# Optimization experiments

Hardware: AMD Instinct MI355X
Metric: run time of the kernel (lower is better)

The kernel has to match this reference:

```python
import jax, jax.numpy as jnp
import numpy as np

N = 50000
E = 800000
IN_F = 128
HID_F = 128
OUT_F = 128
BN_EPS = 1e-5


def make_quaternion_mul(kernel):
    # kernel: [d_in//4, d_out]; returns hamilton: [d_in, d_out]
    r, i, j, k = jnp.split(kernel, 4, axis=1)
    r2 = jnp.concatenate([r, -i, -j, -k], axis=0)
    i2 = jnp.concatenate([i, r, -k, j], axis=0)
    j2 = jnp.concatenate([j, k, r, -i], axis=0)
    k2 = jnp.concatenate([k, -j, i, r], axis=0)
    return jnp.concatenate([r2, i2, j2, k2], axis=1)


def setup_inputs() -> dict:
    key = jax.random.key(0)
    k1, k2, k3, k4, k5, k6 = jax.random.split(key, 6)
    stdv = np.sqrt(6.0 / (IN_F // 4 + HID_F)).astype(np.float32)
    inputs = {
        "input": jax.random.normal(k1, (N, IN_F), dtype=jnp.float32),
        "adj_row": jnp.sort(jax.random.randint(k2, (E,), 0, N, dtype=jnp.int32)),
        "adj_col": jax.random.randint(k3, (E,), 0, N, dtype=jnp.int32),
        "adj_val": jax.random.uniform(k4, (E,), dtype=jnp.float32),
        "weight1": jax.random.uniform(k5, (IN_F // 4, HID_F), minval=-stdv, maxval=stdv, dtype=jnp.float32),
        "weight2": jax.random.uniform(k6, (HID_F // 4, OUT_F), minval=-stdv, maxval=stdv, dtype=jnp.float32),
        "gamma": jnp.ones((OUT_F,), dtype=jnp.float32),
        "beta": jnp.zeros((OUT_F,), dtype=jnp.float32),
    }
    return inputs


def reference(input, adj_row, adj_col, adj_val, weight1, weight2, gamma, beta):
    hamilton1 = make_quaternion_mul(weight1)  # [IN_F, HID_F]
    hamilton2 = make_quaternion_mul(weight2)  # [HID_F, OUT_F]
    out1 = jnp.tanh(input @ hamilton1)        # [N, HID_F]
    out2 = out1 @ hamilton2                   # [N, OUT_F]
    # sparse adj (COO) x dense: out[i] = sum_e val[e] * out2[col[e]] for row[e]==i
    gathered = adj_val[:, None] * out2[adj_col]  # [E, OUT_F]
    agg = jax.ops.segment_sum(gathered, adj_row, num_segments=N)  # [N, OUT_F]
    # BatchNorm1d (training mode): per-feature stats over nodes, biased var
    mean = jnp.mean(agg, axis=0)
    var = jnp.var(agg, axis=0)
    return gamma * (agg - mean) * jax.lax.rsqrt(var + BN_EPS) + beta
```

## Files before the change

kernel.cpp:

```cpp
#include <hip/hip_runtime.h>
#include <cstddef>
#include <cstdint>

#define F 128
#define LDK 136
#define AGG_BLOCKS 2048
#define MID_BLOCKS 64

typedef __attribute__((ext_vector_type(8))) short short8;
typedef __attribute__((ext_vector_type(4))) float f32x4;

__device__ __forceinline__ short f2bf(float f) {
  uint32_t u = __float_as_uint(f);
  uint32_t r = u + 0x7FFFu + ((u >> 16) & 1u);
  return (short)(r >> 16);
}
__device__ __forceinline__ float bf2f(short h) {
  return __uint_as_float(((uint32_t)(uint16_t)h) << 16);
}

__global__ __launch_bounds__(256) void setup_kernel(
    const float* __restrict__ w1, const float* __restrict__ w2,
    short* __restrict__ Hpk, const int* __restrict__ adj_row,
    int* __restrict__ rowptr, int E, int N) {
  if (blockIdx.x < 16) {
    int idx = blockIdx.x * 256 + threadIdx.x;
    int m = idx >> 11;
    int kt = (idx >> 9) & 3;
    int ct = (idx >> 6) & 7;
    int l = idx & 63;
    int col = ct * 16 + (l & 15);
    const float* w = m ? w2 : w1;
    short hi[8], lo[8];
#pragma unroll
    for (int j = 0; j < 8; ++j) {
      int row = kt * 32 + (l >> 4) * 8 + j;
      int rb = row >> 5, cb = col >> 5;
      int neg = (0x284E >> (cb * 4 + rb)) & 1;
      float v = w[(row & 31) * 128 + (rb ^ cb) * 32 + (col & 31)];
      v = neg ? -v : v;
      short h = f2bf(v);
      hi[j] = h;
      lo[j] = f2bf(v - bf2f(h));
    }
    size_t b0 = ((((size_t)m * 2 + 0) * 4 + kt) * 8 + ct) * 64 + l;
    size_t b1 = ((((size_t)m * 2 + 1) * 4 + kt) * 8 + ct) * 64 + l;
    *(short8*)&Hpk[b0 * 8] = *(short8*)hi;
    *(short8*)&Hpk[b1 * 8] = *(short8*)lo;
  } else {
    int e = (blockIdx.x - 16) * 256 + threadIdx.x;
    if (e >= E) return;
    int r = adj_row[e];
    int rprev = (e == 0) ? -1 : adj_row[e - 1];
    for (int q = rprev + 1; q <= r; ++q) rowptr[q] = e;
    if (e == E - 1) {
      for (int q = r + 1; q <= N; ++q) rowptr[q] = E;
    }
  }
}

__global__ __launch_bounds__(256) void gemm_mfma(
    const float* __restrict__ input, const short* __restrict__ Hpk,
    short* __restrict__ out2b, int N) {
  __shared__ short lds[4][16 * LDK];
  const int t = threadIdx.x;
  const int w = t >> 6, l = t & 63;
  const int lr = l & 15, lg = l >> 4;
  const int grow0 = blockIdx.x * 64 + w * 16;
  short* hid = &lds[w][0];

  short8 a1h[4];
  {
    int arow = grow0 + lr;
    if (arow >= N) arow = N - 1;
    const float* xr = &input[(size_t)arow * F];
#pragma unroll
    for (int kt = 0; kt < 4; ++kt) {
      float xv[8];
      *(float4*)&xv[0] = *(const float4*)&xr[kt * 32 + lg * 8];
      *(float4*)&xv[4] = *(const float4*)&xr[kt * 32 + lg * 8 + 4];
#pragma unroll
      for (int j = 0; j < 8; ++j) ((short*)&a1h[kt])[j] = f2bf(xv[j]);
    }
  }

  f32x4 acc[8];
#pragma unroll
  for (int ct = 0; ct < 8; ++ct) acc[ct] = (f32x4){0.f, 0.f, 0.f, 0.f};
#pragma unroll
  for (int kt = 0; kt < 4; ++kt) {
#pragma unroll
    for (int ct = 0; ct < 8; ++ct) {
      short8 bh = *(const short8*)&Hpk[((((size_t)0 * 4 + kt) * 8 + ct) * 64 + l) * 8];
      short8 bl = *(const short8*)&Hpk[((((size_t)1 * 4 + kt) * 8 + ct) * 64 + l) * 8];
      acc[ct] = __builtin_amdgcn_mfma_f32_16x16x32_bf16(a1h[kt], bl, acc[ct], 0, 0, 0);
      acc[ct] = __builtin_amdgcn_mfma_f32_16x16x32_bf16(a1h[kt], bh, acc[ct], 0, 0, 0);
    }
  }

#pragma unroll
  for (int ct = 0; ct < 8; ++ct)
#pragma unroll
    for (int r = 0; r < 4; ++r)
      hid[(lg * 4 + r) * LDK + ct * 16 + lr] = f2bf(tanhf(acc[ct][r]));

  short8 a2h[4];
#pragma unroll
  for (int kt = 0; kt < 4; ++kt)
    a2h[kt] = *(short8*)&hid[lr * LDK + kt * 32 + lg * 8];

#pragma unroll
  for (int ct = 0; ct < 8; ++ct) acc[ct] = (f32x4){0.f, 0.f, 0.f, 0.f};
#pragma unroll
  for (int kt = 0; kt < 4; ++kt) {
#pragma unroll
    for (int ct = 0; ct < 8; ++ct) {
      short8 bh = *(const short8*)&Hpk[((((size_t)2 * 4 + kt) * 8 + ct) * 64 + l) * 8];
      short8 bl = *(const short8*)&Hpk[((((size_t)3 * 4 + kt) * 8 + ct) * 64 + l) * 8];
      acc[ct] = __builtin_amdgcn_mfma_f32_16x16x32_bf16(a2h[kt], bl, acc[ct], 0, 0, 0);
      acc[ct] = __builtin_amdgcn_mfma_f32_16x16x32_bf16(a2h[kt], bh, acc[ct], 0, 0, 0);
    }
  }

#pragma unroll
  for (int ct = 0; ct < 8; ++ct)
#pragma unroll
    for (int r = 0; r < 4; ++r)
      hid[(lg * 4 + r) * LDK + ct * 16 + lr] = f2bf(acc[ct][r]);
#pragma unroll
  for (int i = 0; i < 4; ++i) {
    int chunk = i * 64 + l;
    int row = chunk >> 4, pos = chunk & 15;
    int grow = grow0 + row;
    if (grow < N)
      *(short8*)&out2b[(size_t)grow * F + pos * 8] = *(short8*)&hid[row * LDK + pos * 8];
  }
}

__global__ __launch_bounds__(256) void agg_rows4(
    const uint32_t* __restrict__ out2u,
    const int* __restrict__ rowptr, const int* __restrict__ adj_col,
    const float* __restrict__ adj_val, float* __restrict__ agg,
    float* __restrict__ partials, int N) {
  const int t = threadIdx.x;
  const int w = t >> 6, lane = t & 63;
  const int sub = lane >> 4;
  const int fl = lane & 15;
  const int wid = blockIdx.x * 4 + w;
  const int nw = gridDim.x * 4;
  float ssum[8], ssq[8];
#pragma unroll
  for (int j = 0; j < 8; ++j) { ssum[j] = 0.f; ssq[j] = 0.f; }

  for (int r = wid; r < N; r += nw) {
    const int row = __builtin_amdgcn_readfirstlane(r);
    const int start = rowptr[row];
    const int end = rowptr[row + 1];
    float acc[8];
#pragma unroll
    for (int j = 0; j < 8; ++j) acc[j] = 0.f;

    int e = start;
    for (; e + 16 <= end; e += 16) {
      int c[4]; float v[4]; uint4 u[4];
#pragma unroll
      for (int q = 0; q < 4; ++q) {
        int ee = e + q * 4 + sub;
        c[q] = adj_col[ee];
        v[q] = adj_val[ee];
      }
#pragma unroll
      for (int q = 0; q < 4; ++q)
        u[q] = *(const uint4*)&out2u[(size_t)c[q] * 64 + fl * 4];
#pragma unroll
      for (int q = 0; q < 4; ++q) {
#pragma unroll
        for (int k = 0; k < 4; ++k) {
          uint32_t uu = ((const uint32_t*)&u[q])[k];
          acc[2 * k]     = fmaf(v[q], __uint_as_float(uu << 16), acc[2 * k]);
          acc[2 * k + 1] = fmaf(v[q], __uint_as_float(uu & 0xFFFF0000u), acc[2 * k + 1]);
        }
      }
    }
    for (; e < end; e += 4) {
      int ee = e + sub;
      bool valid = ee < end;
      int c0 = adj_col[valid ? ee : end - 1];
      float v0 = valid ? adj_val[ee] : 0.f;
      uint4 u = *(const uint4*)&out2u[(size_t)c0 * 64 + fl * 4];
#pragma unroll
      for (int k = 0; k < 4; ++k) {
        uint32_t uu = ((const uint32_t*)&u)[k];
        acc[2 * k]     = fmaf(v0, __uint_as_float(uu << 16), acc[2 * k]);
        acc[2 * k + 1] = fmaf(v0, __uint_as_float(uu & 0xFFFF0000u), acc[2 * k + 1]);
      }
    }
#pragma unroll
    for (int j = 0; j < 8; ++j) {
      acc[j] += __shfl_xor(acc[j], 16, 64);
      acc[j] += __shfl_xor(acc[j], 32, 64);
    }
    if (sub == 0) {
      *(float4*)&agg[(size_t)row * F + fl * 8] = make_float4(acc[0], acc[1], acc[2], acc[3]);
      *(float4*)&agg[(size_t)row * F + fl * 8 + 4] = make_float4(acc[4], acc[5], acc[6], acc[7]);
#pragma unroll
      for (int j = 0; j < 8; ++j) {
        ssum[j] += acc[j];
        ssq[j] = fmaf(acc[j], acc[j], ssq[j]);
      }
    }
  }

  __shared__ float ls[4][128];
  __shared__ float lq[4][128];
  if (sub == 0) {
#pragma unroll
    for (int j = 0; j < 8; ++j) {
      ls[w][fl * 8 + j] = ssum[j];
      lq[w][fl * 8 + j] = ssq[j];
    }
  }
  __syncthreads();
  if (t < 128) {
    float S = ls[0][t] + ls[1][t] + ls[2][t] + ls[3][t];
    float Q = lq[0][t] + lq[1][t] + lq[2][t] + lq[3][t];
    float* dst = &partials[(size_t)blockIdx.x * 256];
    dst[t] = S;
    dst[128 + t] = Q;
  }
}

__global__ __launch_bounds__(256) void mid_reduce(
    const float* __restrict__ partials, float* __restrict__ mid, int nb) {
  const int k = blockIdx.x, t = threadIdx.x;
  const int per = nb / MID_BLOCKS;
  float s = 0.f;
#pragma unroll 4
  for (int i = 0; i < per; ++i)
    s += partials[(size_t)(k * per + i) * 256 + t];
  mid[(size_t)k * 256 + t] = s;
}

__global__ __launch_bounds__(256) void finalize_stats3(
    const float* __restrict__ mid, const float* __restrict__ gamma,
    const float* __restrict__ beta, float* __restrict__ ss, float invN) {
  const int t = threadIdx.x;
  float s = 0.f;
#pragma unroll 8
  for (int b = 0; b < MID_BLOCKS; ++b) s += mid[(size_t)b * 256 + t];
  __shared__ float tot[256];
  tot[t] = s;
  __syncthreads();
  if (t < 128) {
    float mean = tot[t] * invN;
    float var = tot[128 + t] * invN - mean * mean;
    float inv = rsqrtf(var + 1e-5f);
    float sc = gamma[t] * inv;
    ss[t] = sc;
    ss[128 + t] = beta[t] - mean * sc;
  }
}

__global__ __launch_bounds__(256) void bn_apply(
    float* __restrict__ out, const float* __restrict__ ss, int total4) {
  int idx = blockIdx.x * 256 + threadIdx.x;
  if (idx >= total4) return;
  int f4 = (idx & 31) * 4;
  float4 v = *(float4*)&out[(size_t)idx * 4];
  float4 sc = *(const float4*)&ss[f4];
  float4 sh = *(const float4*)&ss[128 + f4];
  v.x = fmaf(v.x, sc.x, sh.x);
  v.y = fmaf(v.y, sc.y, sh.y);
  v.z = fmaf(v.z, sc.z, sh.z);
  v.w = fmaf(v.w, sc.w, sh.w);
  *(float4*)&out[(size_t)idx * 4] = v;
}

extern "C" void kernel_launch(void* const* d_in, const int* in_sizes, int n_in,
                              void* d_out, int out_size, void* d_ws, size_t ws_size,
                              hipStream_t stream) {
  (void)n_in; (void)out_size; (void)ws_size;
  const float* input  = (const float*)d_in[0];
  const int*  adj_row = (const int*)d_in[1];
  const int*  adj_col = (const int*)d_in[2];
  const float* adj_val = (const float*)d_in[3];
  const float* w1 = (const float*)d_in[4];
  const float* w2 = (const float*)d_in[5];
  const float* gamma = (const float*)d_in[6];
  const float* beta  = (const float*)d_in[7];
  const int N = in_sizes[0] / F;
  const int E = in_sizes[1];

  char* ws = (char*)d_ws;
  short* Hpk = (short*)(ws);
  float* ss = (float*)(ws + 131072);
  float* partials = (float*)(ws + 132096);
  float* mid = (float*)(ws + 2229248);
  int* rowptr = (int*)(ws + 2294784);
  short* out2b = (short*)(ws + 2499584);
  float* agg = (float*)d_out;

  setup_kernel<<<16 + (E + 255) / 256, 256, 0, stream>>>(w1, w2, Hpk, adj_row, rowptr, E, N);
  gemm_mfma<<<(N + 63) / 64, 256, 0, stream>>>(input, Hpk, out2b, N);
  agg_rows4<<<AGG_BLOCKS, 256, 0, stream>>>(
      (const uint32_t*)out2b, rowptr, adj_col, adj_val, agg, partials, N);
  mid_reduce<<<MID_BLOCKS, 256, 0, stream>>>(partials, mid, AGG_BLOCKS);
  finalize_stats3<<<1, 256, 0, stream>>>(mid, gamma, beta, ss, 1.0f / (float)N);
  bn_apply<<<(N * 32 + 255) / 256, 256, 0, stream>>>(agg, ss, N * 32);
}
```

Baseline: 90.47 us.

## Pack col/val pairs and aggregate two rows per wave for more gather parallelism

The setup kernel now interleaves adj_col and adj_val into one uint2 array, so the aggregation loads each edge's column and value with a single 8-byte read. The aggregation kernel has each wave process two adjacent rows at once, with predicated 16-edge chunks replacing the separate tail loop, which doubles the independent gathers in flight. The agg grid drops from 2048 to 1280 blocks. The costs are an extra pass writing about 6.4 MB of packed data in setup, wasted masked loads when the two rows have different degrees, and higher register pressure.

New measurement: 87.21 us. 3.6% less time.

```diff
diff --git a/kernel.cpp b/kernel.cpp
--- a/kernel.cpp
+++ b/kernel.cpp
@@ -4,7 +4,7 @@
 
 #define F 128
 #define LDK 136
-#define AGG_BLOCKS 2048
+#define AGG_BLOCKS 1280
 #define MID_BLOCKS 64
 
 typedef __attribute__((ext_vector_type(8))) short short8;
@@ -22,7 +22,8 @@
 __global__ __launch_bounds__(256) void setup_kernel(
     const float* __restrict__ w1, const float* __restrict__ w2,
     short* __restrict__ Hpk, const int* __restrict__ adj_row,
-    int* __restrict__ rowptr, int E, int N) {
+    const int* __restrict__ adj_col, const float* __restrict__ adj_val,
+    int* __restrict__ rowptr, uint2* __restrict__ cv, int E, int N) {
   if (blockIdx.x < 16) {
     int idx = blockIdx.x * 256 + threadIdx.x;
     int m = idx >> 11;
@@ -50,6 +51,7 @@
   } else {
     int e = (blockIdx.x - 16) * 256 + threadIdx.x;
     if (e >= E) return;
+    cv[e] = make_uint2((uint32_t)adj_col[e], __float_as_uint(adj_val[e]));
     int r = adj_row[e];
     int rprev = (e == 0) ? -1 : adj_row[e - 1];
     for (int q = rprev + 1; q <= r; ++q) rowptr[q] = e;
@@ -137,76 +139,101 @@
   }
 }
 
-__global__ __launch_bounds__(256) void agg_rows4(
+__global__ __launch_bounds__(256) void agg_rows6(
     const uint32_t* __restrict__ out2u,
-    const int* __restrict__ rowptr, const int* __restrict__ adj_col,
-    const float* __restrict__ adj_val, float* __restrict__ agg,
-    float* __restrict__ partials, int N) {
+    const int* __restrict__ rowptr, const uint2* __restrict__ cv,
+    float* __restrict__ agg, float* __restrict__ partials, int N) {
   const int t = threadIdx.x;
   const int w = t >> 6, lane = t & 63;
   const int sub = lane >> 4;
-  const int fl = lane & 15;
+  const int fl4 = (lane & 15) * 4;
   const int wid = blockIdx.x * 4 + w;
   const int nw = gridDim.x * 4;
   float ssum[8], ssq[8];
 #pragma unroll
   for (int j = 0; j < 8; ++j) { ssum[j] = 0.f; ssq[j] = 0.f; }
 
-  for (int r = wid; r < N; r += nw) {
-    const int row = __builtin_amdgcn_readfirstlane(r);
-    const int start = rowptr[row];
-    const int end = rowptr[row + 1];
-    float acc[8];
-#pragma unroll
-    for (int j = 0; j < 8; ++j) acc[j] = 0.f;
-
-    int e = start;
-    for (; e + 16 <= end; e += 16) {
-      int c[4]; float v[4]; uint4 u[4];
+  for (int pr = wid; pr * 2 < N; pr += nw) {
+    const int rowA = pr * 2;
+    const bool hasB = rowA + 1 < N;
+    const int sA = rowptr[rowA];
+    const int eAe = rowptr[rowA + 1];
+    const int eBe = hasB ? rowptr[rowA + 2] : eAe;
+    const int sB = eAe;
+
+    float accA[8], accB[8];
+#pragma unroll
+    for (int j = 0; j < 8; ++j) { accA[j] = 0.f; accB[j] = 0.f; }
+
+    int eA = sA, eB = sB;
+    while (eA < eAe || eB < eBe) {
+      float vA[4], vB[4];
+      uint32_t cA[4], cB[4];
 #pragma unroll
       for (int q = 0; q < 4; ++q) {
-        int ee = e + q * 4 + sub;
-        c[q] = adj_col[ee];
-        v[q] = adj_val[ee];
-      }
+        int ee = eA + q * 4 + sub;
+        bool val = ee < eAe;
+        int idx = val ? ee : (eAe - 1);
+        idx = idx < 0 ? 0 : idx;
+        uint2 p = cv[idx];
+        cA[q] = p.x;
+        vA[q] = val ? __uint_as_float(p.y) : 0.f;
+      }
+#pragma unroll
+      for (int q = 0; q < 4; ++q) {
+        int ee = eB + q * 4 + sub;
+        bool val = ee < eBe;
+        int idx = val ? ee : (eBe - 1);
+        idx = idx < 0 ? 0 : idx;
+        uint2 p = cv[idx];
+        cB[q] = p.x;
+        vB[q] = val ? __uint_as_float(p.y) : 0.f;
+      }
+      uint4 uA[4], uB[4];
 #pragma unroll
       for (int q = 0; q < 4; ++q)
-        u[q] = *(const uint4*)&out2u[(size_t)c[q] * 64 + fl * 4];
+        uA[q] = *(const uint4*)&out2u[(size_t)(cA[q] * 64u + fl4)];
+#pragma unroll
+      for (int q = 0; q < 4; ++q)
+        uB[q] = *(const uint4*)&out2u[(size_t)(cB[q] * 64u + fl4)];
 #pragma unroll
       for (int q = 0; q < 4; ++q) {
 #pragma unroll
         for (int k = 0; k < 4; ++k) {
-          uint32_t uu = ((const uint32_t*)&u[q])[k];
-          acc[2 * k]     = fmaf(v[q], __uint_as_float(uu << 16), acc[2 * k]);
-          acc[2 * k + 1] = fmaf(v[q], __uint_as_float(uu & 0xFFFF0000u), acc[2 * k + 1]);
+          uint32_t ua = ((const uint32_t*)&uA[q])[k];
+          uint32_t ub = ((const uint32_t*)&uB[q])[k];
+          accA[2 * k]     = fmaf(vA[q], __uint_as_float(ua << 16), accA[2 * k]);
+          accA[2 * k + 1] = fmaf(vA[q], __uint_as_float(ua & 0xFFFF0000u), accA[2 * k + 1]);
+          accB[2 * k]     = fmaf(vB[q], __uint_as_float(ub << 16), accB[2 * k]);
+          accB[2 * k + 1] = fmaf(vB[q], __uint_as_float(ub & 0xFFFF0000u), accB[2 * k + 1]);
         }
       }
-    }
-    for (; e < end; e += 4) {
-      int ee = e + sub;
-      bool valid = ee < end;
-      int c0 = adj_col[valid ? ee : end - 1];
-      float v0 = valid ? adj_val[ee] : 0.f;
-      uint4 u = *(const uint4*)&out2u[(size_t)c0 * 64 + fl * 4];
-#pragma unroll
-      for (int k = 0; k < 4; ++k) {
-        uint32_t uu = ((const uint32_t*)&u)[k];
-        acc[2 * k]     = fmaf(v0, __uint_as_float(uu << 16), acc[2 * k]);
-        acc[2 * k + 1] = fmaf(v0, __uint_as_float(uu & 0xFFFF0000u), acc[2 * k + 1]);
-      }
+      eA += 16;
+      eB += 16;
     }
 #pragma unroll
     for (int j = 0; j < 8; ++j) {
-      acc[j] += __shfl_xor(acc[j], 16, 64);
-      acc[j] += __shfl_xor(acc[j], 32, 64);
+      accA[j] += __shfl_xor(accA[j], 16, 64);
+      accA[j] += __shfl_xor(accA[j], 32, 64);
+      accB[j] += __shfl_xor(accB[j], 16, 64);
+      accB[j] += __shfl_xor(accB[j], 32, 64);
     }
     if (sub == 0) {
-      *(float4*)&agg[(size_t)row * F + fl * 8] = make_float4(acc[0], acc[1], acc[2], acc[3]);
-      *(float4*)&agg[(size_t)row * F + fl * 8 + 4] = make_float4(acc[4], acc[5], acc[6], acc[7]);
+      *(float4*)&agg[(size_t)rowA * F + fl4 * 2] = make_float4(accA[0], accA[1], accA[2], accA[3]);
+      *(float4*)&agg[(size_t)rowA * F + fl4 * 2 + 4] = make_float4(accA[4], accA[5], accA[6], accA[7]);
 #pragma unroll
       for (int j = 0; j < 8; ++j) {
-        ssum[j] += acc[j];
-        ssq[j] = fmaf(acc[j], acc[j], ssq[j]);
+        ssum[j] += accA[j];
+        ssq[j] = fmaf(accA[j], accA[j], ssq[j]);
+      }
+      if (hasB) {
+        *(float4*)&agg[(size_t)(rowA + 1) * F + fl4 * 2] = make_float4(accB[0], accB[1], accB[2], accB[3]);
+        *(float4*)&agg[(size_t)(rowA + 1) * F + fl4 * 2 + 4] = make_float4(accB[4], accB[5], accB[6], accB[7]);
+#pragma unroll
+        for (int j = 0; j < 8; ++j) {
+          ssum[j] += accB[j];
+          ssq[j] = fmaf(accB[j], accB[j], ssq[j]);
+        }
       }
     }
   }
@@ -216,8 +243,8 @@
   if (sub == 0) {
 #pragma unroll
     for (int j = 0; j < 8; ++j) {
-      ls[w][fl * 8 + j] = ssum[j];
-      lq[w][fl * 8 + j] = ssq[j];
+      ls[w][fl4 * 2 + j] = ssum[j];
+      lq[w][fl4 * 2 + j] = ssq[j];
     }
   }
   __syncthreads();
@@ -297,13 +324,16 @@
   float* partials = (float*)(ws + 132096);
   float* mid = (float*)(ws + 2229248);
   int* rowptr = (int*)(ws + 2294784);
-  short* out2b = (short*)(ws + 2499584);
+  uint2* cv = (uint2*)(ws + 2499584);
+  size_t cv_bytes = ((size_t)E * 8 + 511) & ~(size_t)511;
+  short* out2b = (short*)(ws + 2499584 + cv_bytes);
   float* agg = (float*)d_out;
 
-  setup_kernel<<<16 + (E + 255) / 256, 256, 0, stream>>>(w1, w2, Hpk, adj_row, rowptr, E, N);
+  setup_kernel<<<16 + (E + 255) / 256, 256, 0, stream>>>(
+      w1, w2, Hpk, adj_row, adj_col, adj_val, rowptr, cv, E, N);
   gemm_mfma<<<(N + 63) / 64, 256, 0, stream>>>(input, Hpk, out2b, N);
-  agg_rows4<<<AGG_BLOCKS, 256, 0, stream>>>(
-      (const uint32_t*)out2b, rowptr, adj_col, adj_val, agg, partials, N);
+  agg_rows6<<<AGG_BLOCKS, 256, 0, stream>>>(
+      (const uint32_t*)out2b, rowptr, cv, agg, partials, N);
   mid_reduce<<<MID_BLOCKS, 256, 0, stream>>>(partials, mid, AGG_BLOCKS);
   finalize_stats3<<<1, 256, 0, stream>>>(mid, gamma, beta, ss, 1.0f / (float)N);
   bn_apply<<<(N * 32 + 255) / 256, 256, 0, stream>>>(agg, ss, N * 32);
```
